# Kernel tuning notes

Hardware: AMD Instinct MI355X
Metric: run time of the kernel (lower is better)

Reference implementation:

```python
import jax, jax.numpy as jnp
import numpy as np

KH = KW = 3  # deform conv kernel
EPS = 1e-12  # F.normalize eps


def _deform_sample(img, u, v):
    """Flow-guided deformable sampling: bilinear gather of img at each of the
    9 kernel offsets shifted by the per-pixel flow (u=dx, v=dy).
    img: [B,C,H,W]; u,v: [B,1,H,W] -> returns [B,C,9,H,W]."""
    B, C, H, W = img.shape
    ky, kx = jnp.meshgrid(jnp.arange(KH) - 1, jnp.arange(KW) - 1, indexing='ij')
    ky = ky.reshape(1, 9, 1, 1).astype(img.dtype)
    kx = kx.reshape(1, 9, 1, 1).astype(img.dtype)
    iy = jnp.arange(H, dtype=img.dtype).reshape(1, 1, H, 1)
    ix = jnp.arange(W, dtype=img.dtype).reshape(1, 1, 1, W)
    py = iy + ky + v  # [B,9,H,W]
    px = ix + kx + u
    y0 = jnp.floor(py); x0 = jnp.floor(px)
    wy = py - y0; wx = px - x0  # bilinear weights
    y0i = y0.astype(jnp.int32); x0i = x0.astype(jnp.int32)
    flat = img.reshape(B, C, H * W)

    def gather(yi, xi):
        valid = ((yi >= 0) & (yi < H) & (xi >= 0) & (xi < W)).astype(img.dtype)
        idx = jnp.clip(yi, 0, H - 1) * W + jnp.clip(xi, 0, W - 1)  # [B,9,H,W]
        g = jax.vmap(lambda f, i: jnp.take(f, i.reshape(-1), axis=1))(flat, idx)
        return g.reshape(B, C, 9, H, W) * valid[:, None]

    s = (gather(y0i, x0i) * ((1 - wy) * (1 - wx))[:, None]
         + gather(y0i, x0i + 1) * ((1 - wy) * wx)[:, None]
         + gather(y0i + 1, x0i) * (wy * (1 - wx))[:, None]
         + gather(y0i + 1, x0i + 1) * (wy * wx)[:, None])
    return s


def setup_inputs() -> dict:
    key = jax.random.key(0)
    k1, k2, k3, k4, k5 = jax.random.split(key, 5)
    B, C, H, W = 2, 64, 256, 256
    num_heads = 4
    clone = jax.random.normal(k1, (B, C, H, W), dtype=jnp.float32)
    x = jax.random.normal(k2, (B, C, H * W), dtype=jnp.float32)
    u = jax.random.normal(k3, (B, 1, H, W), dtype=jnp.float32)
    v = jax.random.normal(k4, (B, 1, H, W), dtype=jnp.float32)
    weight = jax.random.normal(k5, (C, C, KH, KW), dtype=jnp.float32) * 0.05
    temperature = jnp.ones((num_heads, 1, 1), dtype=jnp.float32)
    return {"clone": clone, "x": x, "u": u, "v": v,
            "weight": weight, "temperature": temperature}


def reference(clone, x, u, v, weight, temperature):
    # deformable conv: bilinear gather then contract over (in_ch, kernel)
    s = _deform_sample(clone, u, v)                      # [B,C,9,H,W]
    w = weight.reshape(weight.shape[0], weight.shape[1], 9)
    conv = jnp.einsum('bckhw,ock->bohw', s, w)           # [B,C,H,W]
    B, C, H, W = conv.shape
    head = temperature.shape[0]
    kv = conv.reshape(B, head, C // head, H * W)          # k = v = deform output
    q = x.reshape(B, head, C // head, H * W)
    qn = q / jnp.maximum(jnp.linalg.norm(q, axis=-1, keepdims=True), EPS)
    kn = kv / jnp.maximum(jnp.linalg.norm(kv, axis=-1, keepdims=True), EPS)
    attn = jnp.einsum('bhcs,bhds->bhcd', qn, kn) * temperature  # [B,h,c,c]
    attn = jax.nn.softmax(attn, axis=-1)
    out = jnp.einsum('bhcd,bhds->bhcs', attn, kv)
    return out.reshape(B, C, H * W)
```

## Files before the change

kernel.cpp:

```cpp
#include <hip/hip_runtime.h>

typedef __bf16 bf16;
typedef __bf16 bf16x4 __attribute__((ext_vector_type(4)));
typedef __bf16 bf16x8 __attribute__((ext_vector_type(8)));
typedef float  f32x4  __attribute__((ext_vector_type(4)));

#define HH 256
#define WW 256
#define NB 2
#define NC 64
#define NS 65536
#define EX 258
#define NHEAD 4
#define DH 16
#define NSTRIPE 8
#define ACCSZ 2304

#define OFF_CEXT   0ul
#define OFF_KV     17040384ul
#define OFF_WPK    33817600ul
#define OFF_ACC    33891328ul

__global__ void k0w(const float* __restrict__ wgt, bf16* __restrict__ wpk,
                    float* __restrict__ accums) {
    int t = blockIdx.x * 256 + threadIdx.x;
    if (t < 9 * 2 * 4 * 64) {
        int L   = t & 63;
        int mtg = (t >> 6) & 3;
        int kc  = (t >> 8) & 1;
        int tap = t >> 9;
        int o  = mtg * 16 + (L & 15);
        int cb = kc * 32 + (L >> 4) * 8;
        bf16x8 vv;
        #pragma unroll
        for (int j = 0; j < 8; j++)
            vv[j] = (bf16)wgt[(o * 64 + (cb + j)) * 9 + tap];
        *(bf16x8*)(wpk + t * 8) = vv;
    }
    int z = t - 9 * 2 * 4 * 64;
    if (z >= 0 && z < NSTRIPE * ACCSZ) accums[z] = 0.0f;
}

__global__ __launch_bounds__(256, 2) void k1_conv(const float* __restrict__ clone,
                                                  const bf16* __restrict__ wpk,
                                                  bf16* __restrict__ cext) {
    const int Xt = blockIdx.x;
    const int Yt = blockIdx.y;
    const int b  = blockIdx.z;
    const int t  = threadIdx.x;
    const int L  = t & 63;
    const int wv = t >> 6;
    const int mpair = wv >> 1;
    const int npair = wv & 1;

    extern __shared__ bf16 tile[];

    bf16x8 afrag[2][9][2];
    #pragma unroll
    for (int mt = 0; mt < 2; mt++)
        #pragma unroll
        for (int tap = 0; tap < 9; tap++)
            #pragma unroll
            for (int kc = 0; kc < 2; kc++) {
                int idx = ((tap * 2 + kc) * 4 + (mpair * 2 + mt)) * 64 + L;
                afrag[mt][tap][kc] = *(const bf16x8*)(wpk + idx * 8);
            }

    for (int u = t; u < 2176; u += 256) {
        int xq = u % 17;
        int rc = u / 17;
        int cg = rc & 15;
        int r  = rc >> 4;
        int y  = Yt * 6 - 2 + r;
        int xg0 = Xt * 64 - 4 + xq * 4;
        int c0 = cg * 4;
        f32x4 f[4];
        bool yin = (y >= 0) && (y < HH);
        if (yin && xg0 >= 0 && xg0 + 3 < WW) {
            #pragma unroll
            for (int i = 0; i < 4; i++)
                f[i] = *(const f32x4*)(clone + ((size_t)(b * NC + c0 + i) * HH + y) * WW + xg0);
        } else {
            #pragma unroll
            for (int i = 0; i < 4; i++)
                #pragma unroll
                for (int e = 0; e < 4; e++) {
                    int xg = xg0 + e;
                    f[i][e] = (yin && xg >= 0 && xg < WW)
                            ? clone[((size_t)(b * NC + c0 + i) * HH + y) * WW + xg] : 0.0f;
                }
        }
        #pragma unroll
        for (int e = 0; e < 4; e++) {
            bf16x4 h;
            #pragma unroll
            for (int i = 0; i < 4; i++) h[i] = (bf16)f[i][e];
            *(bf16x4*)(tile + (r * 68 + xq * 4 + e) * 72 + c0) = h;
        }
    }
    __syncthreads();

    const int nbase = Xt * 64 + npair * 32;
    const f32x4 zero4 = {0.0f, 0.0f, 0.0f, 0.0f};
    for (int Yi = 0; Yi < 6; Yi++) {
        f32x4 acc[2][2];
        acc[0][0] = zero4; acc[0][1] = zero4; acc[1][0] = zero4; acc[1][1] = zero4;
        #pragma unroll
        for (int tap = 0; tap < 9; tap++) {
            const int ky = tap / 3 - 1;
            const int kx = tap % 3 - 1;
            const int r = Yi + 1 + ky;
            #pragma unroll
            for (int kc = 0; kc < 2; kc++) {
                const int cb = kc * 32 + (L >> 4) * 8;
                #pragma unroll
                for (int nt = 0; nt < 2; nt++) {
                    if (nbase + nt * 16 < EX) {
                        const int col = npair * 32 + nt * 16 + (L & 15) + kx + 3;
                        bf16x8 bfrag = *(const bf16x8*)(tile + (r * 68 + col) * 72 + cb);
                        #pragma unroll
                        for (int mt = 0; mt < 2; mt++)
                            acc[mt][nt] = __builtin_amdgcn_mfma_f32_16x16x32_bf16(
                                afrag[mt][tap][kc], bfrag, acc[mt][nt], 0, 0, 0);
                    }
                }
            }
        }
        int Yp = Yt * 6 + Yi;
        #pragma unroll
        for (int mt = 0; mt < 2; mt++)
            #pragma unroll
            for (int nt = 0; nt < 2; nt++) {
                int Xp = Xt * 64 + npair * 32 + nt * 16 + (L & 15);
                if (Xp < EX) {
                    int o = mpair * 32 + mt * 16 + (L >> 4) * 4;
                    bf16x4 st;
                    #pragma unroll
                    for (int rg = 0; rg < 4; rg++) st[rg] = (bf16)acc[mt][nt][rg];
                    *(bf16x4*)(cext + ((((size_t)b * EX + Yp) * EX + Xp) << 6) + o) = st;
                }
            }
    }
}

__global__ __launch_bounds__(256) void k2_gd(const float* __restrict__ uu,
                                             const float* __restrict__ vv,
                                             const float* __restrict__ x,
                                             const bf16* __restrict__ cext,
                                             bf16* __restrict__ kv,
                                             float* __restrict__ accums) {
    const int bx = blockIdx.x;
    const int b  = blockIdx.z;
    const int strip = (bx & 7) * 64 + (bx >> 3);
    const int t = threadIdx.x;
    const int px = t >> 1;
    const int half = t & 1;
    const int hw = strip * 128 + px;
    const int idx = b * NS + hw;
    const int hy = hw >> 8;
    const int wx = hw & 255;

    __shared__ bf16 tile[128][68];

    float fv = vv[idx];
    float fu = uu[idx];
    float py_f = (float)hy + fv;
    float px_f = (float)wx + fu;
    float fy = floorf(py_f);
    float fx = floorf(px_f);
    float ay = py_f - fy;
    float ax = px_f - fx;
    int ys = (int)fy + 1;
    int xs = (int)fx + 1;
    float w00 = (1.0f - ay) * (1.0f - ax);
    float w01 = (1.0f - ay) * ax;
    float w10 = ay * (1.0f - ax);
    float w11 = ay * ax;
    bool y0i = (ys >= 0) && (ys < EX);
    bool y1i = (ys + 1 >= 0) && (ys + 1 < EX);
    bool x0i = (xs >= 0) && (xs < EX);
    bool x1i = (xs + 1 >= 0) && (xs + 1 < EX);
    if (!y0i) { w00 = 0.0f; w01 = 0.0f; }
    if (!y1i) { w10 = 0.0f; w11 = 0.0f; }
    if (!x0i) { w00 = 0.0f; w10 = 0.0f; }
    if (!x1i) { w01 = 0.0f; w11 = 0.0f; }
    int y0c = ys < 0 ? 0 : (ys > EX - 1 ? EX - 1 : ys);
    int y1c = ys + 1 < 0 ? 0 : (ys + 1 > EX - 1 ? EX - 1 : ys + 1);
    int x0c = xs < 0 ? 0 : (xs > EX - 1 ? EX - 1 : xs);
    int x1c = xs + 1 < 0 ? 0 : (xs + 1 > EX - 1 ? EX - 1 : xs + 1);
    const bf16* pb = cext + (((size_t)b * EX * EX) << 6);
    size_t i00 = ((size_t)(y0c * EX + x0c)) << 6;
    size_t i01 = ((size_t)(y0c * EX + x1c)) << 6;
    size_t i10 = ((size_t)(y1c * EX + x0c)) << 6;
    size_t i11 = ((size_t)(y1c * EX + x1c)) << 6;
    const int c0 = half * 32;
    bf16* kvp = kv + (((size_t)(b * NC + c0)) << 16) + hw;
    #pragma unroll
    for (int g = 0; g < 4; g++) {
        int cg = c0 + g * 8;
        bf16x8 c00 = *(const bf16x8*)(pb + i00 + cg);
        bf16x8 c01 = *(const bf16x8*)(pb + i01 + cg);
        bf16x8 c10 = *(const bf16x8*)(pb + i10 + cg);
        bf16x8 c11 = *(const bf16x8*)(pb + i11 + cg);
        bf16x4 lo, hi;
        #pragma unroll
        for (int j = 0; j < 8; j++) {
            float val = w00 * (float)c00[j] + w01 * (float)c01[j]
                      + w10 * (float)c10[j] + w11 * (float)c11[j];
            bf16 hv = (bf16)val;
            if (j < 4) lo[j] = hv; else hi[j - 4] = hv;
            kvp[((size_t)(g * 8 + j)) << 16] = hv;
        }
        *(bf16x4*)(&tile[px][c0 + g * 8])     = lo;
        *(bf16x4*)(&tile[px][c0 + g * 8 + 4]) = hi;
    }
    __syncthreads();

    const int L  = t & 63;
    const int h  = t >> 6;
    const int row = L & 15;
    const int kg  = L >> 4;
    const int bh = b * NHEAD + h;
    const float* qb = x + ((size_t)(b * NC + h * DH + row)) * NS + strip * 128;
    f32x4 acc = {0.0f, 0.0f, 0.0f, 0.0f};
    float qp = 0.0f, kp = 0.0f;
    #pragma unroll
    for (int it = 0; it < 4; it++) {
        const int s = it * 32 + kg * 8;
        f32x4 q0 = *(const f32x4*)(qb + s);
        f32x4 q1 = *(const f32x4*)(qb + s + 4);
        bf16x8 qa, ka;
        #pragma unroll
        for (int j = 0; j < 4; j++) {
            qa[j]     = (bf16)q0[j];
            qa[j + 4] = (bf16)q1[j];
        }
        #pragma unroll
        for (int j = 0; j < 8; j++) ka[j] = tile[s + j][h * DH + row];
        qp += q0[0]*q0[0] + q0[1]*q0[1] + q0[2]*q0[2] + q0[3]*q0[3]
            + q1[0]*q1[0] + q1[1]*q1[1] + q1[2]*q1[2] + q1[3]*q1[3];
        #pragma unroll
        for (int j = 0; j < 8; j++) {
            float kf = (float)ka[j];
            kp += kf * kf;
        }
        acc = __builtin_amdgcn_mfma_f32_16x16x32_bf16(qa, ka, acc, 0, 0, 0);
    }
    float* astripe = accums + (bx & 7) * ACCSZ;
    #pragma unroll
    for (int rg = 0; rg < 4; rg++)
        atomicAdd(astripe + bh * 256 + (kg * 4 + rg) * 16 + row, acc[rg]);
    qp += __shfl_xor(qp, 16); qp += __shfl_xor(qp, 32);
    kp += __shfl_xor(kp, 16); kp += __shfl_xor(kp, 32);
    if (kg == 0) {
        atomicAdd(astripe + 2048 + bh * 16 + row, qp);
        atomicAdd(astripe + 2176 + bh * 16 + row, kp);
    }
}

__global__ __launch_bounds__(256) void k5_out(const bf16* __restrict__ kv,
                                              const float* __restrict__ accums,
                                              const float* __restrict__ temp,
                                              float* __restrict__ out) {
    const int ci = blockIdx.x;
    const int h  = blockIdx.y;
    const int b  = blockIdx.z;
    const int t  = threadIdx.x;
    const int bh = b * NHEAD + h;
    __shared__ float l[256];
    __shared__ float a[256];
    {
        int i = t >> 4, j = t & 15;
        float dsum = 0.0f, q2 = 0.0f, k2 = 0.0f;
        #pragma unroll
        for (int st = 0; st < NSTRIPE; st++) {
            dsum += accums[st * ACCSZ + bh * 256 + t];
            q2   += accums[st * ACCSZ + 2048 + bh * 16 + i];
            k2   += accums[st * ACCSZ + 2176 + bh * 16 + j];
        }
        float qn = fmaxf(sqrtf(q2), 1e-12f);
        float kn = fmaxf(sqrtf(k2), 1e-12f);
        float logit = dsum / (qn * kn) * temp[h];
        l[t] = logit;
        __syncthreads();
        float mx = -1e30f;
        #pragma unroll
        for (int jj = 0; jj < 16; jj++) mx = fmaxf(mx, l[i * 16 + jj]);
        float sum = 0.0f;
        #pragma unroll
        for (int jj = 0; jj < 16; jj++) sum += expf(l[i * 16 + jj] - mx);
        a[t] = expf(logit - mx) / sum;
        __syncthreads();
    }
    const int s = (ci * 256 + t) * 4;
    const bf16* kvb = kv + (((size_t)(b * NC + h * DH)) << 16) + s;
    f32x4 kf[16];
    #pragma unroll
    for (int j = 0; j < 16; j++) {
        bf16x4 kk = *(const bf16x4*)(kvb + ((size_t)j << 16));
        #pragma unroll
        for (int e = 0; e < 4; e++) kf[j][e] = (float)kk[e];
    }
    float* ob = out + ((size_t)(b * NC + h * DH)) * NS + s;
    #pragma unroll
    for (int i = 0; i < 16; i++) {
        f32x4 o = {0.0f, 0.0f, 0.0f, 0.0f};
        #pragma unroll
        for (int j = 0; j < 16; j++)
            o += a[i * 16 + j] * kf[j];
        *(f32x4*)(ob + (size_t)i * NS) = o;
    }
}

extern "C" void kernel_launch(void* const* d_in, const int* in_sizes, int n_in,
                              void* d_out, int out_size, void* d_ws, size_t ws_size,
                              hipStream_t stream) {
    const float* clone = (const float*)d_in[0];
    const float* x     = (const float*)d_in[1];
    const float* u     = (const float*)d_in[2];
    const float* v     = (const float*)d_in[3];
    const float* wgt   = (const float*)d_in[4];
    const float* temp  = (const float*)d_in[5];
    float* out = (float*)d_out;

    char* ws = (char*)d_ws;
    bf16*  cext   = (bf16*) (ws + OFF_CEXT);
    bf16*  kv     = (bf16*) (ws + OFF_KV);
    bf16*  wpk    = (bf16*) (ws + OFF_WPK);
    float* accums = (float*)(ws + OFF_ACC);

    static bool attr_set = false;
    if (!attr_set) {
        hipFuncSetAttribute((const void*)k1_conv,
                            hipFuncAttributeMaxDynamicSharedMemorySize, 78336);
        attr_set = true;
    }

    k0w<<<90, 256, 0, stream>>>(wgt, wpk, accums);
    k1_conv<<<dim3(5, 43, 2), 256, 78336, stream>>>(clone, wpk, cext);
    k2_gd<<<dim3(512, 1, 2), 256, 0, stream>>>(u, v, x, cext, kv, accums);
    k5_out<<<dim3(64, 4, 2), 256, 0, stream>>>(kv, accums, temp, out);
}
```

Baseline: 158.2 us.

## Store kv channel-last and restructure output kernel around pixel strips

The gather kernel now writes kv in a pixel-major, channel-contiguous layout with one 16-byte vector store per 8 channels, replacing the scalar stores strided by 64K elements. The output kernel is reorganised so each block handles a 128-pixel strip across all heads. It computes all four heads' softmax in shared memory, does the attention-times-kv product per pixel, and transposes the result through shared memory for coalesced fp32 output writes. This removes the uncoalesced scattered kv writes, at the cost of redundant softmax work in every block and extra shared-memory traffic.

```diff
diff --git a/kernel.cpp b/kernel.cpp
--- a/kernel.cpp
+++ b/kernel.cpp
@@ -147,7 +147,7 @@
                                              const float* __restrict__ vv,
                                              const float* __restrict__ x,
                                              const bf16* __restrict__ cext,
-                                             bf16* __restrict__ kv,
+                                             bf16* __restrict__ kvT,
                                              float* __restrict__ accums) {
     const int bx = blockIdx.x;
     const int b  = blockIdx.z;
@@ -194,7 +194,7 @@
     size_t i10 = ((size_t)(y1c * EX + x0c)) << 6;
     size_t i11 = ((size_t)(y1c * EX + x1c)) << 6;
     const int c0 = half * 32;
-    bf16* kvp = kv + (((size_t)(b * NC + c0)) << 16) + hw;
+    bf16* kvp = kvT + ((size_t)(b * NS + hw)) * 64 + c0;
     #pragma unroll
     for (int g = 0; g < 4; g++) {
         int cg = c0 + g * 8;
@@ -203,16 +203,18 @@
         bf16x8 c10 = *(const bf16x8*)(pb + i10 + cg);
         bf16x8 c11 = *(const bf16x8*)(pb + i11 + cg);
         bf16x4 lo, hi;
+        bf16x8 sv;
         #pragma unroll
         for (int j = 0; j < 8; j++) {
             float val = w00 * (float)c00[j] + w01 * (float)c01[j]
                       + w10 * (float)c10[j] + w11 * (float)c11[j];
             bf16 hv = (bf16)val;
+            sv[j] = hv;
             if (j < 4) lo[j] = hv; else hi[j - 4] = hv;
-            kvp[((size_t)(g * 8 + j)) << 16] = hv;
-        }
-        *(bf16x4*)(&tile[px][c0 + g * 8])     = lo;
-        *(bf16x4*)(&tile[px][c0 + g * 8 + 4]) = hi;
+        }
+        *(bf16x8*)(kvp + g * 8) = sv;
+        *(bf16x4*)(&tile[px][cg])     = lo;
+        *(bf16x4*)(&tile[px][cg + 4]) = hi;
     }
     __syncthreads();
 
@@ -258,57 +260,100 @@
     }
 }
 
-__global__ __launch_bounds__(256) void k5_out(const bf16* __restrict__ kv,
+__global__ __launch_bounds__(256) void k5_out(const bf16* __restrict__ kvT,
                                               const float* __restrict__ accums,
                                               const float* __restrict__ temp,
                                               float* __restrict__ out) {
-    const int ci = blockIdx.x;
-    const int h  = blockIdx.y;
+    const int bx = blockIdx.x;
     const int b  = blockIdx.z;
-    const int t  = threadIdx.x;
-    const int bh = b * NHEAD + h;
-    __shared__ float l[256];
-    __shared__ float a[256];
+    const int strip = (bx & 7) * 64 + (bx >> 3);
+    const int t = threadIdx.x;
+
+    __shared__ float attn[NHEAD * 256];
+    __shared__ float oT[128 * 68];
+
     {
-        int i = t >> 4, j = t & 15;
-        float dsum = 0.0f, q2 = 0.0f, k2 = 0.0f;
-        #pragma unroll
-        for (int st = 0; st < NSTRIPE; st++) {
-            dsum += accums[st * ACCSZ + bh * 256 + t];
-            q2   += accums[st * ACCSZ + 2048 + bh * 16 + i];
-            k2   += accums[st * ACCSZ + 2176 + bh * 16 + j];
-        }
-        float qn = fmaxf(sqrtf(q2), 1e-12f);
-        float kn = fmaxf(sqrtf(k2), 1e-12f);
-        float logit = dsum / (qn * kn) * temp[h];
-        l[t] = logit;
+        const int i = t >> 4, j = t & 15;
+        float lv[4], mx[4], sm[4];
+        #pragma unroll
+        for (int h = 0; h < NHEAD; h++) {
+            const int bh = b * NHEAD + h;
+            float dsum = 0.0f, q2 = 0.0f, k2v = 0.0f;
+            #pragma unroll
+            for (int st = 0; st < NSTRIPE; st++) {
+                dsum += accums[st * ACCSZ + bh * 256 + t];
+                q2   += accums[st * ACCSZ + 2048 + bh * 16 + i];
+                k2v  += accums[st * ACCSZ + 2176 + bh * 16 + j];
+            }
+            float qn = fmaxf(sqrtf(q2), 1e-12f);
+            float kn = fmaxf(sqrtf(k2v), 1e-12f);
+            lv[h] = dsum / (qn * kn) * temp[h];
+            attn[(h * 16 + j) * 16 + i] = lv[h];
+        }
         __syncthreads();
-        float mx = -1e30f;
-        #pragma unroll
-        for (int jj = 0; jj < 16; jj++) mx = fmaxf(mx, l[i * 16 + jj]);
-        float sum = 0.0f;
-        #pragma unroll
-        for (int jj = 0; jj < 16; jj++) sum += expf(l[i * 16 + jj] - mx);
-        a[t] = expf(logit - mx) / sum;
+        #pragma unroll
+        for (int h = 0; h < NHEAD; h++) {
+            float m = -1e30f;
+            #pragma unroll
+            for (int jj = 0; jj < 16; jj++) m = fmaxf(m, attn[(h * 16 + jj) * 16 + i]);
+            float s = 0.0f;
+            #pragma unroll
+            for (int jj = 0; jj < 16; jj++) s += expf(attn[(h * 16 + jj) * 16 + i] - m);
+            mx[h] = m; sm[h] = s;
+        }
         __syncthreads();
-    }
-    const int s = (ci * 256 + t) * 4;
-    const bf16* kvb = kv + (((size_t)(b * NC + h * DH)) << 16) + s;
-    f32x4 kf[16];
-    #pragma unroll
-    for (int j = 0; j < 16; j++) {
-        bf16x4 kk = *(const bf16x4*)(kvb + ((size_t)j << 16));
-        #pragma unroll
-        for (int e = 0; e < 4; e++) kf[j][e] = (float)kk[e];
-    }
-    float* ob = out + ((size_t)(b * NC + h * DH)) * NS + s;
-    #pragma unroll
-    for (int i = 0; i < 16; i++) {
-        f32x4 o = {0.0f, 0.0f, 0.0f, 0.0f};
-        #pragma unroll
-        for (int j = 0; j < 16; j++)
-            o += a[i * 16 + j] * kf[j];
-        *(f32x4*)(ob + (size_t)i * NS) = o;
+        #pragma unroll
+        for (int h = 0; h < NHEAD; h++)
+            attn[(h * 16 + j) * 16 + i] = expf(lv[h] - mx[h]) / sm[h];
+        __syncthreads();
+    }
+
+    {
+        const int px = t >> 1;
+        const int half = t & 1;
+        const int c0 = half * 32;
+        const int h0 = half * 2;
+        const int hw = strip * 128 + px;
+        const bf16* kr = kvT + ((size_t)(b * NS + hw)) * 64 + c0;
+        float kf[32];
+        #pragma unroll
+        for (int g = 0; g < 4; g++) {
+            bf16x8 kk = *(const bf16x8*)(kr + g * 8);
+            #pragma unroll
+            for (int j = 0; j < 8; j++) kf[g * 8 + j] = (float)kk[j];
+        }
+        f32x4 acc[8];
+        #pragma unroll
+        for (int q = 0; q < 8; q++) acc[q] = (f32x4){0.0f, 0.0f, 0.0f, 0.0f};
+        #pragma unroll
+        for (int hh = 0; hh < 2; hh++)
+            #pragma unroll
+            for (int j = 0; j < 16; j++) {
+                const float kvv = kf[hh * 16 + j];
+                const float* ab = &attn[((h0 + hh) * 16 + j) * 16];
+                #pragma unroll
+                for (int q = 0; q < 4; q++)
+                    acc[hh * 4 + q] += *(const f32x4*)(ab + q * 4) * kvv;
+            }
+        #pragma unroll
+        for (int hh = 0; hh < 2; hh++)
+            #pragma unroll
+            for (int q = 0; q < 4; q++)
+                *(f32x4*)(&oT[px * 68 + c0 + hh * 16 + q * 4]) = acc[hh * 4 + q];
+    }
+    __syncthreads();
+
+    {
+        const int c  = t >> 2;
+        const int sq = t & 3;
+        float* op = out + (((size_t)(b * NC + c)) << 16) + strip * 128 + sq * 32;
+        #pragma unroll
+        for (int e = 0; e < 8; e++) {
+            f32x4 ov;
+            #pragma unroll
+            for (int k = 0; k < 4; k++) ov[k] = oT[(sq * 32 + e * 4 + k) * 68 + c];
+            *(f32x4*)(op + e * 4) = ov;
+        }
     }
 }
 
@@ -325,7 +370,7 @@
 
     char* ws = (char*)d_ws;
     bf16*  cext   = (bf16*) (ws + OFF_CEXT);
-    bf16*  kv     = (bf16*) (ws + OFF_KV);
+    bf16*  kvT    = (bf16*) (ws + OFF_KV);
     bf16*  wpk    = (bf16*) (ws + OFF_WPK);
     float* accums = (float*)(ws + OFF_ACC);
 
@@ -338,6 +383,6 @@
 
     k0w<<<90, 256, 0, stream>>>(wgt, wpk, accums);
     k1_conv<<<dim3(5, 43, 2), 256, 78336, stream>>>(clone, wpk, cext);
-    k2_gd<<<dim3(512, 1, 2), 256, 0, stream>>>(u, v, x, cext, kv, accums);
-    k5_out<<<dim3(64, 4, 2), 256, 0, stream>>>(kv, accums, temp, out);
-}
+    k2_gd<<<dim3(512, 1, 2), 256, 0, stream>>>(u, v, x, cext, kvT, accums);
+    k5_out<<<dim3(512, 1, 2), 256, 0, stream>>>(kvT, accums, temp, out);
+}
```

New measurement: 167.3 us. 1.06x slower.
